# Kernel optimization log

Hardware: AMD Instinct MI355X
Metric: run time of the kernel (lower is better)

The kernel has to match this reference:

```python
import jax, jax.numpy as jnp
import numpy as np

B, C, H, W = 2, 256, 48, 48
M = 16           # num_anchors
NH = 4           # num_heads
HD = C // NH     # head_dim
N = H * W


def setup_inputs() -> dict:
    key = jax.random.key(0)
    ks = jax.random.split(key, 16)
    std = 0.02
    inp = {
        'x': jax.random.normal(ks[0], (B, C, H, W), jnp.float32),
        'phi': jax.random.normal(ks[1], (B, M, H, W), jnp.float32),
        'spatial_mask': jnp.ones((B, 1, H, W), jnp.bool_),
        # qkv / out projections
        'Wq': jax.random.normal(ks[2], (C, C), jnp.float32) * std,
        'bq': jnp.zeros((C,), jnp.float32),
        'Wk': jax.random.normal(ks[3], (C, C), jnp.float32) * std,
        'bk': jnp.zeros((C,), jnp.float32),
        'Wv': jax.random.normal(ks[4], (C, C), jnp.float32) * std,
        'bv': jnp.zeros((C,), jnp.float32),
        'Wo': jax.random.normal(ks[5], (C, C), jnp.float32) * std,
        'bo': jnp.zeros((C,), jnp.float32),
        # geodesic PE MLP: Linear(M, C//2) -> GELU -> Linear(C//2, C)
        'W1': jax.random.normal(ks[6], (C // 2, M), jnp.float32) * std,
        'b1': jnp.zeros((C // 2,), jnp.float32),
        'W2': jax.random.normal(ks[7], (C, C // 2), jnp.float32) * std,
        'b2': jnp.zeros((C,), jnp.float32),
        # kernel / bias params
        'log_alpha': jnp.asarray(0.0, jnp.float32),            # log(1.0)
        'beta': jnp.full((NH,), 0.5, jnp.float32),
    }
    return inp


def reference(x, phi, spatial_mask, Wq, bq, Wk, bk, Wv, bv, Wo, bo,
              W1, b1, W2, b2, log_alpha, beta):
    b, c, h, w = x.shape
    n = h * w
    nh = beta.shape[0]
    hd = c // nh
    scale = hd ** -0.5

    # [B, N, M] multi-anchor embedding per token
    phi_flat = phi.reshape(b, -1, n).transpose(0, 2, 1)

    # geodesic positional encoding (exact GELU, as torch nn.GELU default)
    pe = jax.nn.gelu(phi_flat @ W1.T + b1, approximate=False) @ W2.T + b2  # [B,N,C]
    x_flat = x.reshape(b, c, n).transpose(0, 2, 1) + pe                   # [B,N,C]

    # qkv -> [B, NH, N, HD]
    def split_heads(t):
        return t.reshape(b, n, nh, hd).transpose(0, 2, 1, 3)
    q = split_heads(x_flat @ Wq.T + bq)
    k = split_heads(x_flat @ Wk.T + bk)
    v = split_heads(x_flat @ Wv.T + bv)

    logits = jnp.einsum('bhnd,bhmd->bhnm', q, k) * scale  # [B,NH,N,N]

    # pairwise geodesic log-kernel: -alpha * ||phi_i - phi_j||^2 / sqrt(2M)
    phi_sq = jnp.sum(phi_flat ** 2, axis=-1)              # [B,N]
    pairwise = jnp.clip(
        phi_sq[:, :, None] + phi_sq[:, None, :]
        - 2.0 * jnp.einsum('bnm,bkm->bnk', phi_flat, phi_flat),
        0.0, None)                                        # [B,N,N]
    m_anchors = phi_flat.shape[-1]
    log_k_geo = -jnp.exp(log_alpha) * pairwise / np.sqrt(2 * m_anchors)

    logits = logits + beta[None, :, None, None] * log_k_geo[:, None]

    # spatial mask [B,1,H,W] -> pairwise [B,N,N], True = keep
    mask_flat = spatial_mask.reshape(b, n)                # [B,N]
    mask = mask_flat[:, None, :] & mask_flat[:, :, None]  # [B,N,N]
    logits = jnp.where(mask[:, None], logits, -jnp.inf)

    attn = jax.nn.softmax(logits, axis=-1)                # [B,NH,N,N]
    out = jnp.einsum('bhnm,bhmd->bhnd', attn, v)          # [B,NH,N,HD]
    out = out.transpose(0, 2, 1, 3).reshape(b, n, c)
    out = out @ Wo.T + bo
    return out.transpose(0, 2, 1).reshape(b, c, h, w)
```

## Files before the change

### kernel.cpp

```cpp
#include <hip/hip_runtime.h>
#include <hip/hip_bf16.h>
#include <math.h>

#define BB   2
#define CC   256
#define NT   2304
#define NTOK 4608
#define MM   16
#define NHD  4
#define HD   64
#define NBH  8
#define PARTS 4
#define LOG2E 1.4426950408889634f

typedef unsigned short u16;
typedef __attribute__((ext_vector_type(8))) short short8;
typedef __attribute__((ext_vector_type(4))) float f32x4;
typedef __attribute__((ext_vector_type(16))) float f32x16;

__device__ __forceinline__ float bf2f(u16 u) {
  return __uint_as_float(((unsigned)u) << 16);
}
__device__ __forceinline__ u16 f2bf(float f) {
  unsigned u = __float_as_uint(f);
  unsigned r = 0x7FFFu + ((u >> 16) & 1u);
  return (u16)((u + r) >> 16);
}
__device__ __forceinline__ float ld_any(const void* p, size_t i, int fp32) {
  return fp32 ? ((const float*)p)[i] : bf2f(((const u16*)p)[i]);
}

__device__ __forceinline__ int detect_fp32_block(const unsigned* __restrict__ x) {
  __shared__ int cnt4[4];
  __shared__ int resf;
  int t = threadIdx.x;
  unsigned u = x[t];
  unsigned lo = u & 0xFFFFu;
  unsigned e = (lo >> 7) & 0xFFu;
  bool plausible = (lo == 0u) || (e >= 0x60u && e <= 0x88u);
  unsigned long long m = __ballot(plausible);
  if ((t & 63) == 0) cnt4[t >> 6] = __popcll(m);
  __syncthreads();
  if (t == 0) resf = ((cnt4[0] + cnt4[1] + cnt4[2] + cnt4[3]) < 128) ? 1 : 0;
  __syncthreads();
  return resf;
}

static constexpr size_t OFF_CB2   = 16;
static constexpr size_t OFF_CBQ   = OFF_CB2 + 256;
static constexpr size_t OFF_CBK   = OFF_CBQ + 256;
static constexpr size_t OFF_CBV   = OFF_CBK + 256;
static constexpr size_t OFF_CBO   = OFF_CBV + 256;
static constexpr size_t OFF_CLA   = OFF_CBO + 256;
static constexpr size_t OFF_CBETA = OFF_CLA + 16;
static constexpr size_t OFF_WQF   = 1344;
static constexpr size_t OFF_WKF   = OFF_WQF + 32768;
static constexpr size_t OFF_WVF   = OFF_WKF + 32768;
static constexpr size_t OFF_WOF   = OFF_WVF + 32768;
static constexpr size_t OFF_W2F   = OFF_WOF + 32768;
static constexpr size_t OFF_QAUG  = OFF_W2F + 16384;
static constexpr size_t OFF_KAUG  = OFF_QAUG + 1179648;
static constexpr size_t OFF_V3    = OFF_KAUG + 1179648;
static constexpr size_t OFF_OPART = OFF_V3 + 589824;
static constexpr size_t OFF_LPART = OFF_OPART + 2359296;

__global__ __launch_bounds__(256) void setup_kernel(
    const void* __restrict__ x_raw,
    const void* __restrict__ Wq_r, const void* __restrict__ Wk_r,
    const void* __restrict__ Wv_r, const void* __restrict__ Wo_r,
    const void* __restrict__ W2_r,
    const void* __restrict__ b2_r, const void* __restrict__ bq_r,
    const void* __restrict__ bk_r, const void* __restrict__ bv_r,
    const void* __restrict__ bo_r, const void* __restrict__ la_r,
    const void* __restrict__ beta_r,
    float* __restrict__ ws, short* __restrict__ ws16, int* __restrict__ flagp) {
  const int fp32 = detect_fp32_block((const unsigned*)x_raw);
  const int bid = blockIdx.x, t = threadIdx.x;
  if (bid == 0 && t == 0) *flagp = fp32;
  if (bid < 1152) {
    int idx = bid * 256 + t;
    const void* srcs[5] = {Wq_r, Wk_r, Wv_r, Wo_r, W2_r};
    const int elems[5] = {65536, 65536, 65536, 65536, 32768};
    const int ksh[5] = {8, 8, 8, 8, 7};
    const size_t dsts[5] = {OFF_WQF * 2, OFF_WKF * 2, OFF_WVF * 2, OFF_WOF * 2, OFF_W2F * 2};
    int m = 0, off = idx;
    while (off >= elems[m]) { off -= elems[m]; ++m; }
    int ks = ksh[m];
    int n = off >> ks, k = off & ((1 << ks) - 1);
    float v = ld_any(srcs[m], off, fp32);
    ws16[dsts[m] + ((size_t)(k >> 3) * 256 + n) * 8 + (k & 7)] = (short)f2bf(v);
  } else {
    int idx = (bid - 1152) * 256 + t;
    const void* srcs[7] = {b2_r, bq_r, bk_r, bv_r, bo_r, la_r, beta_r};
    const int sizes[7] = {256, 256, 256, 256, 256, 1, 4};
    const int dsts[7] = {(int)OFF_CB2, (int)OFF_CBQ, (int)OFF_CBK, (int)OFF_CBV,
                         (int)OFF_CBO, (int)OFF_CLA, (int)OFF_CBETA};
    if (idx < 1285) {
      int seg = 0, off = idx;
      while (off >= sizes[seg]) { off -= sizes[seg]; ++seg; }
      ws[(size_t)dsts[seg] + off] = ld_any(srcs[seg], off, fp32);
    }
  }
}

__global__ __launch_bounds__(256) void fused_prep(
    const void* __restrict__ x_raw, const void* __restrict__ phi_raw,
    const void* __restrict__ W1_r, const void* __restrict__ b1_r,
    const int* __restrict__ flagp,
    const short* __restrict__ wqf, const short* __restrict__ wkf,
    const short* __restrict__ wvf, const short* __restrict__ w2f,
    const float* __restrict__ bq, const float* __restrict__ bk,
    const float* __restrict__ bv, const float* __restrict__ b2,
    const float* __restrict__ la, const float* __restrict__ beta,
    short* __restrict__ Qaug, short* __restrict__ Kaug, short* __restrict__ V3) {
  __shared__ float phis[16][66];
  __shared__ float phisq_s[64];
  __shared__ float w1s[2048];
  __shared__ float b1s[128];
  __shared__ short hid[16][66][8];
  __shared__ short xfs[32][66][8];

  const int fp32 = *flagp;
  const int t = threadIdx.x;
  const int n0 = blockIdx.x * 64;
  const int b = (n0 >= NT) ? 1 : 0;
  const int nb0 = n0 - b * NT;

  #pragma unroll
  for (int i = 0; i < 4; ++i) {
    int idx = i * 256 + t;
    int m = idx >> 6, j = idx & 63;
    phis[m][j] = ld_any(phi_raw, ((size_t)(b * 16 + m)) * NT + nb0 + j, fp32);
  }
  #pragma unroll
  for (int i = 0; i < 8; ++i) w1s[i * 256 + t] = ld_any(W1_r, i * 256 + t, fp32);
  if (t < 128) b1s[t] = ld_any(b1_r, t, fp32);
  __syncthreads();

  if (t < 64) {
    float s = 0.f;
    #pragma unroll
    for (int m = 0; m < 16; ++m) { float p = phis[m][t]; s += p * p; }
    phisq_s[t] = s;
  }
  {
    const int tok = t & 63, qtr = t >> 6;
    float pr[16];
    #pragma unroll
    for (int m = 0; m < 16; ++m) pr[m] = phis[m][tok];
    #pragma unroll
    for (int cc = 0; cc < 4; ++cc) {
      union { u16 a[8]; short8 v; } pk;
      #pragma unroll
      for (int s8 = 0; s8 < 8; ++s8) {
        int c = qtr * 32 + cc * 8 + s8;
        float acc = b1s[c];
        #pragma unroll
        for (int m = 0; m < 16; ++m) acc += pr[m] * w1s[c * 16 + m];
        float g = 0.5f * acc * (1.f + erff(acc * 0.70710678118654752f));
        pk.a[s8] = f2bf(g);
      }
      *(short8*)&hid[qtr * 4 + cc][tok][0] = pk.v;
    }
  }
  __syncthreads();

  const int lane = t & 63, w = t >> 6;
  const int c32 = lane & 31, H = lane >> 5;
  const int tt = w & 1, chgrp = w >> 1;

  #pragma unroll
  for (int j = 0; j < 4; ++j) {
    const int ch0 = (chgrp * 4 + j) * 32;
    f32x16 acc;
    #pragma unroll
    for (int r = 0; r < 16; ++r) acc[r] = 0.f;
    #pragma unroll
    for (int s = 0; s < 8; ++s) {
      short8 a = *(const short8*)&hid[2 * s + H][tt * 32 + c32][0];
      short8 bb = *(const short8*)&w2f[((size_t)(2 * s + H) * 256 + ch0 + c32) * 8];
      acc = __builtin_amdgcn_mfma_f32_32x32x16_bf16(a, bb, acc, 0, 0, 0);
    }
    const int ch = ch0 + c32;
    const float bias = b2[ch];
    #pragma unroll
    for (int g = 0; g < 4; ++g) {
      int tok0 = tt * 32 + 8 * g + 4 * H;
      size_t xoff = ((size_t)(b * CC + ch)) * NT + nb0 + tok0;
      float4 xv;
      if (fp32) {
        xv = *(const float4*)&((const float*)x_raw)[xoff];
      } else {
        ushort4 xu = *(const ushort4*)&((const u16*)x_raw)[xoff];
        xv = make_float4(bf2f(xu.x), bf2f(xu.y), bf2f(xu.z), bf2f(xu.w));
      }
      float vals[4] = {xv.x, xv.y, xv.z, xv.w};
      #pragma unroll
      for (int e = 0; e < 4; ++e) {
        float v = acc[4 * g + e] + bias + vals[e];
        xfs[ch >> 3][tok0 + e][ch & 7] = (short)f2bf(v);
      }
    }
  }
  __syncthreads();

  #pragma unroll
  for (int z = 0; z < 3; ++z) {
    const short* wf = (z == 0) ? wqf : (z == 1) ? wkf : wvf;
    const float* bias = (z == 0) ? bq : (z == 1) ? bk : bv;
    const float sc = (z == 0) ? 0.125f * LOG2E : 1.f;
    #pragma unroll
    for (int j = 0; j < 4; ++j) {
      const int ch0 = (chgrp * 4 + j) * 32;
      f32x16 acc;
      #pragma unroll
      for (int r = 0; r < 16; ++r) acc[r] = 0.f;
      #pragma unroll
      for (int s = 0; s < 16; ++s) {
        short8 a = *(const short8*)&xfs[2 * s + H][tt * 32 + c32][0];
        short8 bb = *(const short8*)&wf[((size_t)(2 * s + H) * 256 + ch0 + c32) * 8];
        acc = __builtin_amdgcn_mfma_f32_32x32x16_bf16(a, bb, acc, 0, 0, 0);
      }
      const int ch = ch0 + c32;
      const int h = ch >> 6, chh = ch & 63;
      const int bh = b * NHD + h;
      const float bv_ = bias[ch];
      if (z < 2) {
        short* dst = (z == 0) ? Qaug : Kaug;
        const int kq = chh >> 3, sub = chh & 7;
        #pragma unroll
        for (int r = 0; r < 16; ++r) {
          int tok = tt * 32 + (r & 3) + 8 * (r >> 2) + 4 * H;
          int nloc = nb0 + tok;
          dst[((size_t)(bh * 16 + kq) * NT + nloc) * 8 + sub] =
              (short)f2bf((acc[r] + bv_) * sc);
        }
      } else {
        const int d = chh;
        #pragma unroll
        for (int r = 0; r < 16; ++r) {
          int tok = tt * 32 + (r & 3) + 8 * (r >> 2) + 4 * H;
          int n = nb0 + tok;
          int chunk = (n >> 6) * 8 + ((n >> 5) & 1) * 4 + ((n >> 4) & 1) * 2 + ((n >> 2) & 1);
          int jj = (n & 3) + 4 * ((n >> 3) & 1);
          V3[((size_t)(bh * 288 + chunk) * 64 + d) * 8 + jj] = (short)f2bf(acc[r] + bv_);
        }
      }
    }
  }

  {
    const int tok = t & 63, h = t >> 6;
    const int bh = b * NHD + h;
    const int n = nb0 + tok;
    float coef = -__expf(la[0]) * beta[h] * 0.17677669529663687f * LOG2E;
    float s2c = -2.f * coef;
    u16 sflip = (s2c < 0.f) ? 0x8000u : 0u;
    float s = sqrtf(fabsf(s2c));
    u16 qh[16], ql[16];
    #pragma unroll
    for (int m = 0; m < MM; ++m) {
      float v = s * phis[m][tok];
      u16 hv = f2bf(v);
      qh[m] = hv;
      ql[m] = f2bf(v - bf2f(hv));
    }
    float cp = coef * phisq_s[tok];
    u16 chi = f2bf(cp);
    u16 clo = f2bf(cp - bf2f(chi));
    union { u16 a[8]; short8 v; } ch;
    auto wr = [&](short* dst, int kq) {
      *(short8*)&dst[((size_t)(bh * 16 + kq) * NT + n) * 8] = ch.v;
    };
    #pragma unroll
    for (int p = 0; p < 8; ++p) ch.a[p] = qh[p];      wr(Qaug, 8);
    #pragma unroll
    for (int p = 0; p < 8; ++p) ch.a[p] = qh[8 + p];  wr(Qaug, 9);
    #pragma unroll
    for (int p = 0; p < 8; ++p) ch.a[p] = ql[p];      wr(Qaug, 10);
    #pragma unroll
    for (int p = 0; p < 8; ++p) ch.a[p] = ql[8 + p];  wr(Qaug, 11);
    #pragma unroll
    for (int p = 0; p < 8; ++p) ch.a[p] = qh[p];      wr(Qaug, 12);
    #pragma unroll
    for (int p = 0; p < 8; ++p) ch.a[p] = qh[8 + p];  wr(Qaug, 13);
    #pragma unroll
    for (int p = 0; p < 8; ++p) ch.a[p] = 0;
    ch.a[0] = 0x3F80u; ch.a[1] = 0x3F80u;             wr(Qaug, 14);
    ch.a[0] = 0; ch.a[1] = 0;                         wr(Qaug, 15);
    #pragma unroll
    for (int p = 0; p < 8; ++p) ch.a[p] = qh[p] ? (u16)(qh[p] ^ sflip) : (u16)0;      wr(Kaug, 8);
    #pragma unroll
    for (int p = 0; p < 8; ++p) ch.a[p] = qh[8+p] ? (u16)(qh[8+p] ^ sflip) : (u16)0;  wr(Kaug, 9);
    #pragma unroll
    for (int p = 0; p < 8; ++p) ch.a[p] = qh[p] ? (u16)(qh[p] ^ sflip) : (u16)0;      wr(Kaug, 10);
    #pragma unroll
    for (int p = 0; p < 8; ++p) ch.a[p] = qh[8+p] ? (u16)(qh[8+p] ^ sflip) : (u16)0;  wr(Kaug, 11);
    #pragma unroll
    for (int p = 0; p < 8; ++p) ch.a[p] = ql[p] ? (u16)(ql[p] ^ sflip) : (u16)0;      wr(Kaug, 12);
    #pragma unroll
    for (int p = 0; p < 8; ++p) ch.a[p] = ql[8+p] ? (u16)(ql[8+p] ^ sflip) : (u16)0;  wr(Kaug, 13);
    #pragma unroll
    for (int p = 0; p < 8; ++p) ch.a[p] = 0;
    ch.a[0] = chi; ch.a[1] = clo;                     wr(Kaug, 14);
    ch.a[0] = 0; ch.a[1] = 0;                         wr(Kaug, 15);
  }
}

__global__ __launch_bounds__(256) void attn_v3(
    const short* __restrict__ Qaug, const short* __restrict__ Kaug,
    const short* __restrict__ V3,
    u16* __restrict__ opart, float* __restrict__ lpart) {
  __shared__ float omrg[2][2][16][64];
  __shared__ float lmrg[64];
  const int t = threadIdx.x, lane = t & 63, w = t >> 6;
  const int qh = w >> 1, kh = w & 1;
  const int c32 = lane & 31, H = lane >> 5;
  const int qt = blockIdx.x, bh = blockIdx.y, part = blockIdx.z;
  const int q0 = qt * 64;
  const int qrow = q0 + qh * 32 + c32;

  const short* qbase = Qaug + (size_t)bh * 16 * NT * 8;
  const short* kbase = Kaug + (size_t)bh * 16 * NT * 8;
  const short* vbase = V3 + (size_t)bh * 288 * 64 * 8;

  short8 qf[8];
  #pragma unroll
  for (int s = 0; s < 8; ++s)
    qf[s] = *(const short8*)&qbase[((size_t)(2 * s + H) * NT + qrow) * 8];

  f32x16 o[2];
  #pragma unroll
  for (int nt = 0; nt < 2; ++nt)
    #pragma unroll
    for (int r = 0; r < 16; ++r) o[nt][r] = 0.f;
  float lsum = 0.f;

  const int kt0 = part * 9;
  short8 kf[2][8], vf[2][4];
  {
    int j = kt0 * 64 + kh * 32 + c32;
    #pragma unroll
    for (int s = 0; s < 8; ++s)
      kf[0][s] = *(const short8*)&kbase[((size_t)(2 * s + H) * NT + j) * 8];
    #pragma unroll
    for (int st = 0; st < 2; ++st)
      #pragma unroll
      for (int nt = 0; nt < 2; ++nt)
        vf[0][st * 2 + nt] = *(const short8*)&vbase[
            ((size_t)(kt0 * 8 + kh * 4 + st * 2 + H) * 64 + nt * 32 + c32) * 8];
  }

  #pragma unroll
  for (int it = 0; it < 9; ++it) {
    const int cur = it & 1, nxt = cur ^ 1;
    if (it < 8) {
      int ktn = kt0 + it + 1;
      int jn = ktn * 64 + kh * 32 + c32;
      #pragma unroll
      for (int s = 0; s < 8; ++s)
        kf[nxt][s] = *(const short8*)&kbase[((size_t)(2 * s + H) * NT + jn) * 8];
      #pragma unroll
      for (int st = 0; st < 2; ++st)
        #pragma unroll
        for (int nt = 0; nt < 2; ++nt)
          vf[nxt][st * 2 + nt] = *(const short8*)&vbase[
              ((size_t)(ktn * 8 + kh * 4 + st * 2 + H) * 64 + nt * 32 + c32) * 8];
    }

    f32x16 s0, s1;
    #pragma unroll
    for (int r = 0; r < 16; ++r) { s0[r] = 0.f; s1[r] = 0.f; }
    #pragma unroll
    for (int s = 0; s < 4; ++s)
      s0 = __builtin_amdgcn_mfma_f32_32x32x16_bf16(kf[cur][s], qf[s], s0, 0, 0, 0);
    #pragma unroll
    for (int s = 4; s < 8; ++s)
      s1 = __builtin_amdgcn_mfma_f32_32x32x16_bf16(kf[cur][s], qf[s], s1, 0, 0, 0);

    float p[16];
    #pragma unroll
    for (int r = 0; r < 16; ++r) { p[r] = exp2f(s0[r] + s1[r]); lsum += p[r]; }

    short8 pf[2];
    #pragma unroll
    for (int st = 0; st < 2; ++st) {
      union { unsigned u[4]; short8 v; } pk;
      #pragma unroll
      for (int j2 = 0; j2 < 4; ++j2) {
        __hip_bfloat162 hh = __float22bfloat162_rn(
            make_float2(p[8 * st + 2 * j2], p[8 * st + 2 * j2 + 1]));
        pk.u[j2] = *(unsigned*)&hh;
      }
      pf[st] = pk.v;
    }

    #pragma unroll
    for (int st = 0; st < 2; ++st)
      #pragma unroll
      for (int nt = 0; nt < 2; ++nt)
        o[nt] = __builtin_amdgcn_mfma_f32_32x32x16_bf16(pf[st], vf[cur][st * 2 + nt],
                                                        o[nt], 0, 0, 0);
  }

  lsum += __shfl_xor(lsum, 32, 64);

  if (kh == 1) {
    #pragma unroll
    for (int nt = 0; nt < 2; ++nt)
      #pragma unroll
      for (int r = 0; r < 16; ++r) omrg[qh][nt][r][lane] = o[nt][r];
    if (H == 0) lmrg[qh * 32 + c32] = lsum;
  }
  __syncthreads();
  if (kh == 0) {
    float lt = lsum + lmrg[qh * 32 + c32];
    u16* ob = opart + ((size_t)(part * NBH + bh)) * NT * 64;
    #pragma unroll
    for (int nt = 0; nt < 2; ++nt)
      #pragma unroll
      for (int r = 0; r < 16; ++r) {
        float v = o[nt][r] + omrg[qh][nt][r][lane];
        int row = q0 + qh * 32 + (r & 3) + 8 * (r >> 2) + 4 * H;
        ob[(size_t)row * 64 + nt * 32 + c32] = f2bf(v);
      }
    if (H == 0)
      lpart[((size_t)(part * NBH + bh)) * NT + q0 + qh * 32 + c32] = lt;
  }
}

__global__ __launch_bounds__(256) void merge_oproj(
    const u16* __restrict__ opart, const float* __restrict__ lpart,
    const short* __restrict__ wof, const float* __restrict__ bo,
    void* __restrict__ outp, const int* __restrict__ flagp) {
  __shared__ short afragB[32][66][8];
  const int fp32 = *flagp;
  const int t = threadIdx.x;
  const int n0 = blockIdx.x * 64;
  const int b = (n0 >= NT) ? 1 : 0;
  const int nb0 = n0 - b * NT;

  #pragma unroll 4
  for (int i = 0; i < 64; ++i) {
    int idx = i * 256 + t;
    int d = idx & 63, tok = (idx >> 6) & 63, h = idx >> 12;
    int bh = b * NHD + h, n = nb0 + tok;
    float os = 0.f, ls = 0.f;
    #pragma unroll
    for (int p = 0; p < PARTS; ++p) {
      os += bf2f(opart[((size_t)(p * NBH + bh) * NT + n) * 64 + d]);
      ls += lpart[(size_t)(p * NBH + bh) * NT + n];
    }
    int c = h * 64 + d;
    afragB[c >> 3][tok][c & 7] = (short)f2bf(os / ls);
  }
  __syncthreads();

  const int lane = t & 63, w = t >> 6;
  const int c32 = lane & 31, H = lane >> 5;
  const int tt = w & 1, chgrp = w >> 1;
  #pragma unroll
  for (int j = 0; j < 4; ++j) {
    const int ch0 = (chgrp * 4 + j) * 32;
    f32x16 acc;
    #pragma unroll
    for (int r = 0; r < 16; ++r) acc[r] = 0.f;
    #pragma unroll
    for (int s = 0; s < 16; ++s) {
      short8 a = *(const short8*)&wof[((size_t)(2 * s + H) * 256 + ch0 + c32) * 8];
      short8 bb = *(const short8*)&afragB[2 * s + H][tt * 32 + c32][0];
      acc = __builtin_amdgcn_mfma_f32_32x32x16_bf16(a, bb, acc, 0, 0, 0);
    }
    #pragma unroll
    for (int r = 0; r < 16; ++r) {
      int co = ch0 + (r & 3) + 8 * (r >> 2) + 4 * H;
      float v = acc[r] + bo[co];
      size_t off = ((size_t)(b * CC + co)) * NT + nb0 + tt * 32 + c32;
      if (fp32) ((float*)outp)[off] = v;
      else      ((u16*)outp)[off] = f2bf(v);
    }
  }
}

extern "C" void kernel_launch(void* const* d_in, const int* in_sizes, int n_in,
                              void* d_out, int out_size, void* d_ws, size_t ws_size,
                              hipStream_t stream) {
  float* ws = (float*)d_ws;
  short* ws16 = (short*)d_ws;
  int* flag = (int*)d_ws;

  float* cb2 = ws + OFF_CB2;
  float* cbq = ws + OFF_CBQ; float* cbk = ws + OFF_CBK; float* cbv = ws + OFF_CBV;
  float* cbo = ws + OFF_CBO; float* cla = ws + OFF_CLA; float* cbeta = ws + OFF_CBETA;
  short* wqf = ws16 + OFF_WQF * 2;
  short* wkf = ws16 + OFF_WKF * 2;
  short* wvf = ws16 + OFF_WVF * 2;
  short* wof = ws16 + OFF_WOF * 2;
  short* w2f = ws16 + OFF_W2F * 2;
  short* qaug = ws16 + OFF_QAUG * 2;
  short* kaug = ws16 + OFF_KAUG * 2;
  short* v3   = ws16 + OFF_V3 * 2;
  u16*   opart = (u16*)(ws16 + OFF_OPART * 2);
  float* lpart = ws + OFF_LPART;

  setup_kernel<<<1158, 256, 0, stream>>>(
      d_in[0], d_in[3], d_in[5], d_in[7], d_in[9], d_in[13],
      d_in[14], d_in[4], d_in[6], d_in[8], d_in[10], d_in[15], d_in[16],
      ws, ws16, flag);
  fused_prep<<<72, 256, 0, stream>>>(
      d_in[0], d_in[1], d_in[11], d_in[12], flag,
      wqf, wkf, wvf, w2f, cbq, cbk, cbv, cb2, cla, cbeta,
      qaug, kaug, v3);
  attn_v3<<<dim3(36, 8, PARTS), 256, 0, stream>>>(qaug, kaug, v3, opart, lpart);
  merge_oproj<<<72, 256, 0, stream>>>(opart, lpart, wof, cbo, d_out, flag);
}
```

Before: 177.5 us.

## Split prep into parallel kernels and replace split-K attention with in-block reduction

The monolithic 72-block prep kernel becomes two kernels: a PE/x-fusion kernel over a (72,4) channel-group grid that writes xf to a workspace buffer, and a QKV projection kernel over (72,4,4) blocks that also builds the augmented geodesic columns. This spreads work that ran on only 72 workgroups across many more blocks. Attention moves from 4 key partitions with a separate merge to one 512-thread block per query tile whose 4 key-split waves reduce in LDS and write normalized output directly. That removes the opart/lpart round trip, so the output projection becomes a plain GEMM over a (72,4) grid. In exchange, attention has only 288 blocks with longer serial loops, and there is an extra global write and read of xf.

```diff
diff --git a/kernel.cpp b/kernel.cpp
--- a/kernel.cpp
+++ b/kernel.cpp
@@ -10,7 +10,6 @@
 #define NHD  4
 #define HD   64
 #define NBH  8
-#define PARTS 4
 #define LOG2E 1.4426950408889634f
 
 typedef unsigned short u16;
@@ -34,12 +33,12 @@
   __shared__ int cnt4[4];
   __shared__ int resf;
   int t = threadIdx.x;
-  unsigned u = x[t];
+  unsigned u = x[t & 255];
   unsigned lo = u & 0xFFFFu;
   unsigned e = (lo >> 7) & 0xFFu;
   bool plausible = (lo == 0u) || (e >= 0x60u && e <= 0x88u);
   unsigned long long m = __ballot(plausible);
-  if ((t & 63) == 0) cnt4[t >> 6] = __popcll(m);
+  if ((t & 63) == 0 && (t >> 6) < 4) cnt4[t >> 6] = __popcll(m);
   __syncthreads();
   if (t == 0) resf = ((cnt4[0] + cnt4[1] + cnt4[2] + cnt4[3]) < 128) ? 1 : 0;
   __syncthreads();
@@ -58,11 +57,13 @@
 static constexpr size_t OFF_WVF   = OFF_WKF + 32768;
 static constexpr size_t OFF_WOF   = OFF_WVF + 32768;
 static constexpr size_t OFF_W2F   = OFF_WOF + 32768;
-static constexpr size_t OFF_QAUG  = OFF_W2F + 16384;
+static constexpr size_t OFF_XFB   = OFF_W2F + 16384;
+static constexpr size_t OFF_QAUG  = OFF_XFB + 589824;
 static constexpr size_t OFF_KAUG  = OFF_QAUG + 1179648;
 static constexpr size_t OFF_V3    = OFF_KAUG + 1179648;
-static constexpr size_t OFF_OPART = OFF_V3 + 589824;
-static constexpr size_t OFF_LPART = OFF_OPART + 2359296;
+static constexpr size_t OFF_PHIF  = OFF_V3 + 589824;
+static constexpr size_t OFF_PHISQ = OFF_PHIF + 73728;
+static constexpr size_t OFF_AFRAG = OFF_PHISQ + 4608;
 
 __global__ __launch_bounds__(256) void setup_kernel(
     const void* __restrict__ x_raw,
@@ -103,26 +104,22 @@
   }
 }
 
-__global__ __launch_bounds__(256) void fused_prep(
+__global__ __launch_bounds__(256) void prep_xf(
     const void* __restrict__ x_raw, const void* __restrict__ phi_raw,
     const void* __restrict__ W1_r, const void* __restrict__ b1_r,
     const int* __restrict__ flagp,
-    const short* __restrict__ wqf, const short* __restrict__ wkf,
-    const short* __restrict__ wvf, const short* __restrict__ w2f,
-    const float* __restrict__ bq, const float* __restrict__ bk,
-    const float* __restrict__ bv, const float* __restrict__ b2,
-    const float* __restrict__ la, const float* __restrict__ beta,
-    short* __restrict__ Qaug, short* __restrict__ Kaug, short* __restrict__ V3) {
+    const short* __restrict__ w2f, const float* __restrict__ b2,
+    float* __restrict__ phif, float* __restrict__ phisq,
+    short* __restrict__ xfb) {
   __shared__ float phis[16][66];
   __shared__ float phisq_s[64];
   __shared__ float w1s[2048];
   __shared__ float b1s[128];
   __shared__ short hid[16][66][8];
-  __shared__ short xfs[32][66][8];
 
   const int fp32 = *flagp;
   const int t = threadIdx.x;
-  const int n0 = blockIdx.x * 64;
+  const int n0 = blockIdx.x * 64, cg = blockIdx.y;
   const int b = (n0 >= NT) ? 1 : 0;
   const int nb0 = n0 - b * NT;
 
@@ -142,6 +139,15 @@
     #pragma unroll
     for (int m = 0; m < 16; ++m) { float p = phis[m][t]; s += p * p; }
     phisq_s[t] = s;
+    if (cg == 0) phisq[n0 + t] = s;
+  }
+  if (cg == 0) {
+    #pragma unroll
+    for (int i = 0; i < 4; ++i) {
+      int idx = i * 256 + t;
+      int j = idx >> 4, m = idx & 15;
+      phif[(size_t)(n0 + j) * 16 + m] = phis[m][j];
+    }
   }
   {
     const int tok = t & 63, qtr = t >> 6;
@@ -167,92 +173,56 @@
 
   const int lane = t & 63, w = t >> 6;
   const int c32 = lane & 31, H = lane >> 5;
-  const int tt = w & 1, chgrp = w >> 1;
-
-  #pragma unroll
-  for (int j = 0; j < 4; ++j) {
-    const int ch0 = (chgrp * 4 + j) * 32;
-    f32x16 acc;
-    #pragma unroll
-    for (int r = 0; r < 16; ++r) acc[r] = 0.f;
-    #pragma unroll
-    for (int s = 0; s < 8; ++s) {
-      short8 a = *(const short8*)&hid[2 * s + H][tt * 32 + c32][0];
-      short8 bb = *(const short8*)&w2f[((size_t)(2 * s + H) * 256 + ch0 + c32) * 8];
-      acc = __builtin_amdgcn_mfma_f32_32x32x16_bf16(a, bb, acc, 0, 0, 0);
-    }
-    const int ch = ch0 + c32;
-    const float bias = b2[ch];
-    #pragma unroll
-    for (int g = 0; g < 4; ++g) {
-      int tok0 = tt * 32 + 8 * g + 4 * H;
-      size_t xoff = ((size_t)(b * CC + ch)) * NT + nb0 + tok0;
-      float4 xv;
-      if (fp32) {
-        xv = *(const float4*)&((const float*)x_raw)[xoff];
-      } else {
-        ushort4 xu = *(const ushort4*)&((const u16*)x_raw)[xoff];
-        xv = make_float4(bf2f(xu.x), bf2f(xu.y), bf2f(xu.z), bf2f(xu.w));
-      }
-      float vals[4] = {xv.x, xv.y, xv.z, xv.w};
-      #pragma unroll
-      for (int e = 0; e < 4; ++e) {
-        float v = acc[4 * g + e] + bias + vals[e];
-        xfs[ch >> 3][tok0 + e][ch & 7] = (short)f2bf(v);
-      }
-    }
-  }
-  __syncthreads();
-
-  #pragma unroll
-  for (int z = 0; z < 3; ++z) {
-    const short* wf = (z == 0) ? wqf : (z == 1) ? wkf : wvf;
-    const float* bias = (z == 0) ? bq : (z == 1) ? bk : bv;
-    const float sc = (z == 0) ? 0.125f * LOG2E : 1.f;
-    #pragma unroll
-    for (int j = 0; j < 4; ++j) {
-      const int ch0 = (chgrp * 4 + j) * 32;
-      f32x16 acc;
-      #pragma unroll
-      for (int r = 0; r < 16; ++r) acc[r] = 0.f;
-      #pragma unroll
-      for (int s = 0; s < 16; ++s) {
-        short8 a = *(const short8*)&xfs[2 * s + H][tt * 32 + c32][0];
-        short8 bb = *(const short8*)&wf[((size_t)(2 * s + H) * 256 + ch0 + c32) * 8];
-        acc = __builtin_amdgcn_mfma_f32_32x32x16_bf16(a, bb, acc, 0, 0, 0);
-      }
-      const int ch = ch0 + c32;
-      const int h = ch >> 6, chh = ch & 63;
-      const int bh = b * NHD + h;
-      const float bv_ = bias[ch];
-      if (z < 2) {
-        short* dst = (z == 0) ? Qaug : Kaug;
-        const int kq = chh >> 3, sub = chh & 7;
-        #pragma unroll
-        for (int r = 0; r < 16; ++r) {
-          int tok = tt * 32 + (r & 3) + 8 * (r >> 2) + 4 * H;
-          int nloc = nb0 + tok;
-          dst[((size_t)(bh * 16 + kq) * NT + nloc) * 8 + sub] =
-              (short)f2bf((acc[r] + bv_) * sc);
-        }
-      } else {
-        const int d = chh;
-        #pragma unroll
-        for (int r = 0; r < 16; ++r) {
-          int tok = tt * 32 + (r & 3) + 8 * (r >> 2) + 4 * H;
-          int n = nb0 + tok;
-          int chunk = (n >> 6) * 8 + ((n >> 5) & 1) * 4 + ((n >> 4) & 1) * 2 + ((n >> 2) & 1);
-          int jj = (n & 3) + 4 * ((n >> 3) & 1);
-          V3[((size_t)(bh * 288 + chunk) * 64 + d) * 8 + jj] = (short)f2bf(acc[r] + bv_);
-        }
-      }
-    }
-  }
-
-  {
-    const int tok = t & 63, h = t >> 6;
-    const int bh = b * NHD + h;
-    const int n = nb0 + tok;
+  const int tt = w & 1, chh = w >> 1;
+  const int ch0 = cg * 64 + chh * 32;
+  f32x16 acc;
+  #pragma unroll
+  for (int r = 0; r < 16; ++r) acc[r] = 0.f;
+  #pragma unroll
+  for (int s = 0; s < 8; ++s) {
+    short8 a = *(const short8*)&hid[2 * s + H][tt * 32 + c32][0];
+    short8 bb = *(const short8*)&w2f[((size_t)(2 * s + H) * 256 + ch0 + c32) * 8];
+    acc = __builtin_amdgcn_mfma_f32_32x32x16_bf16(a, bb, acc, 0, 0, 0);
+  }
+  const int ch = ch0 + c32;
+  const float bias = b2[ch];
+  #pragma unroll
+  for (int g = 0; g < 4; ++g) {
+    int tok0 = tt * 32 + 8 * g + 4 * H;
+    size_t xoff = ((size_t)(b * CC + ch)) * NT + nb0 + tok0;
+    float4 xv;
+    if (fp32) {
+      xv = *(const float4*)&((const float*)x_raw)[xoff];
+    } else {
+      ushort4 xu = *(const ushort4*)&((const u16*)x_raw)[xoff];
+      xv = make_float4(bf2f(xu.x), bf2f(xu.y), bf2f(xu.z), bf2f(xu.w));
+    }
+    float vals[4] = {xv.x, xv.y, xv.z, xv.w};
+    #pragma unroll
+    for (int e = 0; e < 4; ++e) {
+      float v = acc[4 * g + e] + bias + vals[e];
+      int gtok = n0 + tok0 + e;
+      xfb[((size_t)(ch >> 3) * NTOK + gtok) * 8 + (ch & 7)] = (short)f2bf(v);
+    }
+  }
+}
+
+__global__ __launch_bounds__(256) void qkv_aug(
+    const short* __restrict__ xfb,
+    const short* __restrict__ wqf, const short* __restrict__ wkf,
+    const short* __restrict__ wvf,
+    const float* __restrict__ bq, const float* __restrict__ bk,
+    const float* __restrict__ bv,
+    const float* __restrict__ phif, const float* __restrict__ phisq,
+    const float* __restrict__ la, const float* __restrict__ beta,
+    short* __restrict__ Qaug, short* __restrict__ Kaug, short* __restrict__ V3) {
+  const int z = blockIdx.z;
+  if (z == 3) {
+    if (blockIdx.y != 0) return;
+    int idx = blockIdx.x * 256 + threadIdx.x;
+    if (idx >= NBH * NT) return;
+    int bh = idx / NT, n = idx - bh * NT;
+    int b = bh >> 2, h = bh & 3;
     float coef = -__expf(la[0]) * beta[h] * 0.17677669529663687f * LOG2E;
     float s2c = -2.f * coef;
     u16 sflip = (s2c < 0.f) ? 0x8000u : 0u;
@@ -260,12 +230,12 @@
     u16 qh[16], ql[16];
     #pragma unroll
     for (int m = 0; m < MM; ++m) {
-      float v = s * phis[m][tok];
+      float v = s * phif[(size_t)(b * NT + n) * MM + m];
       u16 hv = f2bf(v);
       qh[m] = hv;
       ql[m] = f2bf(v - bf2f(hv));
     }
-    float cp = coef * phisq_s[tok];
+    float cp = coef * phisq[b * NT + n];
     u16 chi = f2bf(cp);
     u16 clo = f2bf(cp - bf2f(chi));
     union { u16 a[8]; short8 v; } ch;
@@ -304,21 +274,75 @@
     for (int p = 0; p < 8; ++p) ch.a[p] = 0;
     ch.a[0] = chi; ch.a[1] = clo;                     wr(Kaug, 14);
     ch.a[0] = 0; ch.a[1] = 0;                         wr(Kaug, 15);
-  }
-}
-
-__global__ __launch_bounds__(256) void attn_v3(
+    return;
+  }
+
+  const short* wf = (z == 0) ? wqf : (z == 1) ? wkf : wvf;
+  const float* bias = (z == 0) ? bq : (z == 1) ? bk : bv;
+  const int t = threadIdx.x, lane = t & 63, w = t >> 6;
+  const int col = lane & 15, quad = lane >> 4;
+  const int t0 = blockIdx.x * 64, head = blockIdx.y, c0 = head * 64;
+  const int b = (t0 >= NT) ? 1 : 0;
+  const int arow = t0 + w * 16 + col;
+  f32x4 acc[4];
+  #pragma unroll
+  for (int ct = 0; ct < 4; ++ct) acc[ct] = (f32x4){0.f, 0.f, 0.f, 0.f};
+  #pragma unroll
+  for (int c = 0; c < 8; ++c) {
+    short8 af = *(const short8*)&xfb[((size_t)(c * 4 + quad) * NTOK + arow) * 8];
+    #pragma unroll
+    for (int ct = 0; ct < 4; ++ct) {
+      short8 bfr = *(const short8*)&wf[((size_t)(c * 4 + quad) * 256 + c0 + ct * 16 + col) * 8];
+      acc[ct] = __builtin_amdgcn_mfma_f32_16x16x32_bf16(af, bfr, acc[ct], 0, 0, 0);
+    }
+  }
+  const int r0 = t0 + w * 16 + quad * 4;
+  const int n0l = r0 - b * NT;
+  const int bh = b * NHD + head;
+  if (z < 2) {
+    short* dst = (z == 0) ? Qaug : Kaug;
+    const float sc = (z == 0) ? 0.125f * LOG2E : 1.f;
+    #pragma unroll
+    for (int ct = 0; ct < 4; ++ct) {
+      int chh = ct * 16 + col;
+      float bb = bias[c0 + chh];
+      int kq = chh >> 3, sub = chh & 7;
+      #pragma unroll
+      for (int reg = 0; reg < 4; ++reg) {
+        float v = (acc[ct][reg] + bb) * sc;
+        dst[((size_t)(bh * 16 + kq) * NT + n0l + reg) * 8 + sub] = (short)f2bf(v);
+      }
+    }
+  } else {
+    #pragma unroll
+    for (int ct = 0; ct < 4; ++ct) {
+      int d = ct * 16 + col;
+      float bb = bias[c0 + d];
+      #pragma unroll
+      for (int reg = 0; reg < 4; ++reg) {
+        int n = n0l + reg;
+        int chunk = (n >> 6) * 8 + ((n >> 5) & 1) * 4 + ((n >> 4) & 1) * 2 + ((n >> 2) & 1);
+        int jj = (n & 3) + 4 * ((n >> 3) & 1);
+        V3[((size_t)(bh * 288 + chunk) * 64 + d) * 8 + jj] = (short)f2bf(acc[ct][reg] + bb);
+      }
+    }
+  }
+}
+
+__global__ __launch_bounds__(512) void attn_v4(
     const short* __restrict__ Qaug, const short* __restrict__ Kaug,
-    const short* __restrict__ V3,
-    u16* __restrict__ opart, float* __restrict__ lpart) {
-  __shared__ float omrg[2][2][16][64];
-  __shared__ float lmrg[64];
+    const short* __restrict__ V3, short* __restrict__ afrag) {
+  __shared__ float obuf[2][2][2][16][64];
+  __shared__ float lbuf[2][2][32];
+  __shared__ float lfin[2][32];
+
   const int t = threadIdx.x, lane = t & 63, w = t >> 6;
-  const int qh = w >> 1, kh = w & 1;
+  const int qh = w >> 2, kh = w & 3;
   const int c32 = lane & 31, H = lane >> 5;
-  const int qt = blockIdx.x, bh = blockIdx.y, part = blockIdx.z;
+  const int qt = blockIdx.x, bh = blockIdx.y;
   const int q0 = qt * 64;
   const int qrow = q0 + qh * 32 + c32;
+  const int bg = bh >> 2, hh = bh & 3;
 
   const short* qbase = Qaug + (size_t)bh * 16 * NT * 8;
   const short* kbase = Kaug + (size_t)bh * 16 * NT * 8;
@@ -336,36 +360,36 @@
     for (int r = 0; r < 16; ++r) o[nt][r] = 0.f;
   float lsum = 0.f;
 
-  const int kt0 = part * 9;
   short8 kf[2][8], vf[2][4];
   {
-    int j = kt0 * 64 + kh * 32 + c32;
+    int j = kh * 32 + c32;
     #pragma unroll
     for (int s = 0; s < 8; ++s)
       kf[0][s] = *(const short8*)&kbase[((size_t)(2 * s + H) * NT + j) * 8];
+    int cb = (kh >> 1) * 8 + (kh & 1) * 4;
     #pragma unroll
     for (int st = 0; st < 2; ++st)
       #pragma unroll
       for (int nt = 0; nt < 2; ++nt)
         vf[0][st * 2 + nt] = *(const short8*)&vbase[
-            ((size_t)(kt0 * 8 + kh * 4 + st * 2 + H) * 64 + nt * 32 + c32) * 8];
-  }
-
-  #pragma unroll
-  for (int it = 0; it < 9; ++it) {
+            ((size_t)(cb + st * 2 + H) * 64 + nt * 32 + c32) * 8];
+  }
+
+  #pragma unroll
+  for (int it = 0; it < 18; ++it) {
     const int cur = it & 1, nxt = cur ^ 1;
-    if (it < 8) {
-      int ktn = kt0 + it + 1;
-      int jn = ktn * 64 + kh * 32 + c32;
+    if (it < 17) {
+      int jn = (it + 1) * 128 + kh * 32 + c32;
       #pragma unroll
       for (int s = 0; s < 8; ++s)
         kf[nxt][s] = *(const short8*)&kbase[((size_t)(2 * s + H) * NT + jn) * 8];
+      int cb = ((it + 1) * 2 + (kh >> 1)) * 8 + (kh & 1) * 4;
       #pragma unroll
       for (int st = 0; st < 2; ++st)
         #pragma unroll
         for (int nt = 0; nt < 2; ++nt)
           vf[nxt][st * 2 + nt] = *(const short8*)&vbase[
-              ((size_t)(ktn * 8 + kh * 4 + st * 2 + H) * 64 + nt * 32 + c32) * 8];
+              ((size_t)(cb + st * 2 + H) * 64 + nt * 32 + c32) * 8];
     }
 
     f32x16 s0, s1;
@@ -388,9 +412,9 @@
       union { unsigned u[4]; short8 v; } pk;
       #pragma unroll
       for (int j2 = 0; j2 < 4; ++j2) {
-        __hip_bfloat162 hh = __float22bfloat162_rn(
+        __hip_bfloat162 hh2 = __float22bfloat162_rn(
             make_float2(p[8 * st + 2 * j2], p[8 * st + 2 * j2 + 1]));
-        pk.u[j2] = *(unsigned*)&hh;
+        pk.u[j2] = *(unsigned*)&hh2;
       }
       pf[st] = pk.v;
     }
@@ -405,80 +429,90 @@
 
   lsum += __shfl_xor(lsum, 32, 64);
 
+  if (kh >= 2) {
+    #pragma unroll
+    for (int nt = 0; nt < 2; ++nt)
+      #pragma unroll
+      for (int r = 0; r < 16; ++r) obuf[qh][kh - 2][nt][r][lane] = o[nt][r];
+    if (H == 0) lbuf[qh][kh - 2][c32] = lsum;
+  }
+  __syncthreads();
+  if (kh < 2) {
+    #pragma unroll
+    for (int nt = 0; nt < 2; ++nt)
+      #pragma unroll
+      for (int r = 0; r < 16; ++r) o[nt][r] += obuf[qh][kh][nt][r][lane];
+    lsum += lbuf[qh][kh][c32];
+  }
+  __syncthreads();
   if (kh == 1) {
     #pragma unroll
     for (int nt = 0; nt < 2; ++nt)
       #pragma unroll
-      for (int r = 0; r < 16; ++r) omrg[qh][nt][r][lane] = o[nt][r];
-    if (H == 0) lmrg[qh * 32 + c32] = lsum;
+      for (int r = 0; r < 16; ++r) obuf[qh][1][nt][r][lane] = o[nt][r];
+    if (H == 0) lbuf[qh][1][c32] = lsum;
   }
   __syncthreads();
   if (kh == 0) {
-    float lt = lsum + lmrg[qh * 32 + c32];
-    u16* ob = opart + ((size_t)(part * NBH + bh)) * NT * 64;
     #pragma unroll
     for (int nt = 0; nt < 2; ++nt)
       #pragma unroll
+      for (int r = 0; r < 16; ++r) o[nt][r] += obuf[qh][1][nt][r][lane];
+    lsum += lbuf[qh][1][c32];
+    if (H == 0) lfin[qh][c32] = lsum;
+  }
+  __syncthreads();
+  if (kh == 0) {
+    float4 linv[4];
+    #pragma unroll
+    for (int g = 0; g < 4; ++g) {
+      float4 lv = *(const float4*)&lfin[qh][8 * g + 4 * H];
+      linv[g] = make_float4(1.f / lv.x, 1.f / lv.y, 1.f / lv.z, 1.f / lv.w);
+    }
+    #pragma unroll
+    for (int nt = 0; nt < 2; ++nt) {
+      int c = hh * 64 + nt * 32 + c32;
+      size_t cbase = (size_t)(c >> 3) * NTOK * 8 + (c & 7);
+      #pragma unroll
       for (int r = 0; r < 16; ++r) {
-        float v = o[nt][r] + omrg[qh][nt][r][lane];
-        int row = q0 + qh * 32 + (r & 3) + 8 * (r >> 2) + 4 * H;
-        ob[(size_t)row * 64 + nt * 32 + c32] = f2bf(v);
+        float inv = (r & 3) == 0 ? linv[r >> 2].x : (r & 3) == 1 ? linv[r >> 2].y
+                  : (r & 3) == 2 ? linv[r >> 2].z : linv[r >> 2].w;
+        int n = q0 + qh * 32 + (r & 3) + 8 * (r >> 2) + 4 * H;
+        afrag[cbase + (size_t)(bg * NT + n) * 8] = (short)f2bf(o[nt][r] * inv);
       }
-    if (H == 0)
-      lpart[((size_t)(part * NBH + bh)) * NT + q0 + qh * 32 + c32] = lt;
-  }
-}
-
-__global__ __launch_bounds__(256) void merge_oproj(
-    const u16* __restrict__ opart, const float* __restrict__ lpart,
-    const short* __restrict__ wof, const float* __restrict__ bo,
-    void* __restrict__ outp, const int* __restrict__ flagp) {
-  __shared__ short afragB[32][66][8];
+    }
+  }
+}
+
+__global__ __launch_bounds__(256) void oproj4(
+    const short* __restrict__ afrag, const short* __restrict__ wof,
+    const float* __restrict__ bo, void* __restrict__ outp,
+    const int* __restrict__ flagp) {
   const int fp32 = *flagp;
-  const int t = threadIdx.x;
-  const int n0 = blockIdx.x * 64;
-  const int b = (n0 >= NT) ? 1 : 0;
-  const int nb0 = n0 - b * NT;
-
-  #pragma unroll 4
-  for (int i = 0; i < 64; ++i) {
-    int idx = i * 256 + t;
-    int d = idx & 63, tok = (idx >> 6) & 63, h = idx >> 12;
-    int bh = b * NHD + h, n = nb0 + tok;
-    float os = 0.f, ls = 0.f;
-    #pragma unroll
-    for (int p = 0; p < PARTS; ++p) {
-      os += bf2f(opart[((size_t)(p * NBH + bh) * NT + n) * 64 + d]);
-      ls += lpart[(size_t)(p * NBH + bh) * NT + n];
-    }
-    int c = h * 64 + d;
-    afragB[c >> 3][tok][c & 7] = (short)f2bf(os / ls);
-  }
-  __syncthreads();
-
-  const int lane = t & 63, w = t >> 6;
+  const int t = threadIdx.x, lane = t & 63, w = t >> 6;
   const int c32 = lane & 31, H = lane >> 5;
-  const int tt = w & 1, chgrp = w >> 1;
-  #pragma unroll
-  for (int j = 0; j < 4; ++j) {
-    const int ch0 = (chgrp * 4 + j) * 32;
-    f32x16 acc;
-    #pragma unroll
-    for (int r = 0; r < 16; ++r) acc[r] = 0.f;
-    #pragma unroll
-    for (int s = 0; s < 16; ++s) {
-      short8 a = *(const short8*)&wof[((size_t)(2 * s + H) * 256 + ch0 + c32) * 8];
-      short8 bb = *(const short8*)&afragB[2 * s + H][tt * 32 + c32][0];
-      acc = __builtin_amdgcn_mfma_f32_32x32x16_bf16(a, bb, acc, 0, 0, 0);
-    }
-    #pragma unroll
-    for (int r = 0; r < 16; ++r) {
-      int co = ch0 + (r & 3) + 8 * (r >> 2) + 4 * H;
-      float v = acc[r] + bo[co];
-      size_t off = ((size_t)(b * CC + co)) * NT + nb0 + tt * 32 + c32;
-      if (fp32) ((float*)outp)[off] = v;
-      else      ((u16*)outp)[off] = f2bf(v);
-    }
+  const int t0 = blockIdx.x * 64, cg = blockIdx.y;
+  const int b = (t0 >= NT) ? 1 : 0;
+  const int nb0 = t0 - b * NT;
+  const int tt = w & 1, chh = w >> 1;
+  const int ch0 = cg * 64 + chh * 32;
+
+  f32x16 acc;
+  #pragma unroll
+  for (int r = 0; r < 16; ++r) acc[r] = 0.f;
+  #pragma unroll
+  for (int s = 0; s < 16; ++s) {
+    short8 a = *(const short8*)&wof[((size_t)(2 * s + H) * 256 + ch0 + c32) * 8];
+    short8 bb = *(const short8*)&afrag[((size_t)(2 * s + H) * NTOK + t0 + tt * 32 + c32) * 8];
+    acc = __builtin_amdgcn_mfma_f32_32x32x16_bf16(a, bb, acc, 0, 0, 0);
+  }
+  #pragma unroll
+  for (int r = 0; r < 16; ++r) {
+    int co = ch0 + (r & 3) + 8 * (r >> 2) + 4 * H;
+    float v = acc[r] + bo[co];
+    size_t off = ((size_t)(b * CC + co)) * NT + nb0 + tt * 32 + c32;
+    if (fp32) ((float*)outp)[off] = v;
+    else      ((u16*)outp)[off] = f2bf(v);
   }
 }
 
@@ -492,25 +526,27 @@
   float* cb2 = ws + OFF_CB2;
   float* cbq = ws + OFF_CBQ; float* cbk = ws + OFF_CBK; float* cbv = ws + OFF_CBV;
   float* cbo = ws + OFF_CBO; float* cla = ws + OFF_CLA; float* cbeta = ws + OFF_CBETA;
+  float* phif = ws + OFF_PHIF; float* phisq = ws + OFF_PHISQ;
   short* wqf = ws16 + OFF_WQF * 2;
   short* wkf = ws16 + OFF_WKF * 2;
   short* wvf = ws16 + OFF_WVF * 2;
   short* wof = ws16 + OFF_WOF * 2;
   short* w2f = ws16 + OFF_W2F * 2;
+  short* xfb = ws16 + OFF_XFB * 2;
   short* qaug = ws16 + OFF_QAUG * 2;
   short* kaug = ws16 + OFF_KAUG * 2;
   short* v3   = ws16 + OFF_V3 * 2;
-  u16*   opart = (u16*)(ws16 + OFF_OPART * 2);
-  float* lpart = ws + OFF_LPART;
+  short* afrag = ws16 + OFF_AFRAG * 2;
 
   setup_kernel<<<1158, 256, 0, stream>>>(
       d_in[0], d_in[3], d_in[5], d_in[7], d_in[9], d_in[13],
       d_in[14], d_in[4], d_in[6], d_in[8], d_in[10], d_in[15], d_in[16],
       ws, ws16, flag);
-  fused_prep<<<72, 256, 0, stream>>>(
-      d_in[0], d_in[1], d_in[11], d_in[12], flag,
-      wqf, wkf, wvf, w2f, cbq, cbk, cbv, cb2, cla, cbeta,
-      qaug, kaug, v3);
-  attn_v3<<<dim3(36, 8, PARTS), 256, 0, stream>>>(qaug, kaug, v3, opart, lpart);
-  merge_oproj<<<72, 256, 0, stream>>>(opart, lpart, wof, cbo, d_out, flag);
-}
+  prep_xf<<<dim3(72, 4), 256, 0, stream>>>(
+      d_in[0], d_in[1], d_in[11], d_in[12], flag, w2f, cb2, phif, phisq, xfb);
+  qkv_aug<<<dim3(72, 4, 4), 256, 0, stream>>>(xfb, wqf, wkf, wvf, cbq, cbk, cbv,
+                                              phif, phisq, cla, cbeta,
+                                              qaug, kaug, v3);
+  attn_v4<<<dim3(36, 8), 512, 0, stream>>>(qaug, kaug, v3, afrag);
+  oproj4<<<dim3(72, 4), 256, 0, stream>>>(afrag, wof, cbo, d_out, flag);
+}
```

New measurement: 157.8 us. -11.1%, faster.
